# Kernel optimization log

Measured on AMD Instinct MI355X. Metric: run time of the kernel, lower is better.

The kernel has to match this reference:

```python
import jax, jax.numpy as jnp
import numpy as np

V = 8192
E = 262144
IN_DIM = 128
OUT_DIM = 128
NEG_SLOPE = 0.2


def setup_inputs() -> dict:
    key = jax.random.key(0)
    k1, k2, k3, k4 = jax.random.split(key, 4)
    h = jax.random.normal(k1, (V, IN_DIM), dtype=jnp.float32)
    edge_index = jax.random.randint(k2, (2, E), 0, V, dtype=jnp.int64)
    # nn.Linear weights: W (out_dim, in_dim), att (1, 2*out_dim), both bias-free
    W = jax.random.normal(k3, (OUT_DIM, IN_DIM), dtype=jnp.float32) / np.sqrt(IN_DIM)
    att_w = jax.random.normal(k4, (1, 2 * OUT_DIM), dtype=jnp.float32) / np.sqrt(2 * OUT_DIM)
    return {"h": h, "edge_index": edge_index, "W": W, "att_w": att_w}


def reference(h, edge_index, W, att_w):
    # h: (V, in_dim) -> (V, out_dim)
    hw = h @ W.T
    src, dst = edge_index[0], edge_index[1]
    # edge features: concat of endpoint embeddings -> (E, 2*out_dim)
    e = jnp.concatenate([hw[src], hw[dst]], axis=-1)
    # attention logits per edge, LeakyReLU(0.2)
    a = jax.nn.leaky_relu(jnp.squeeze(e @ att_w.T, -1), negative_slope=NEG_SLOPE)
    v = hw.shape[0]
    # faithful to original: dense V x V matrix, zeros on non-edges,
    # softmax over ALL columns (non-edges included as score 0)
    alpha = jnp.zeros((v, v), dtype=hw.dtype).at[src, dst].set(a)
    alpha = jax.nn.softmax(alpha, axis=-1)
    # dropout is identity in eval mode (deterministic reference)
    return alpha @ hw
```

## Files before the change

kernel.cpp:

```cpp
#include <hip/hip_runtime.h>
#include <hip/hip_bf16.h>
#include <math.h>


#define V 8192
#define E 262144
#define D 128
#define NEG_SLOPE 0.2f
#define CAP 96
#define CSTRIDE 16
#define HWB 512

#define FMA4(acc, hv, wv) { acc.x += (hv)*(wv).x; acc.y += (hv)*(wv).y; \
                            acc.z += (hv)*(wv).z; acc.w += (hv)*(wv).w; }

__device__ __forceinline__ unsigned short f2bf(float f) {
    unsigned u = __float_as_uint(f);
    return (unsigned short)((u + 0x7fffu + ((u >> 16) & 1u)) >> 16);
}
__device__ __forceinline__ float bf2f_low(int p) {
    return __uint_as_float(((unsigned)p) << 16);
}

__global__ __launch_bounds__(256) void k_hw(const float* __restrict__ h,
                                            const float* __restrict__ W,
                                            const float* __restrict__ att,
                                            unsigned short* __restrict__ hwb,
                                            float* __restrict__ s1,
                                            float* __restrict__ s2,
                                            float* __restrict__ Pb,
                                            int* __restrict__ cnt) {
    __shared__ float Wt[D * 132];
    __shared__ float atts[2 * D];
    __shared__ float scr[8 * D];
    int t = threadIdx.x, b = blockIdx.x;
    int g = b * 256 + t;
    cnt[g] = 0;
    atts[t] = att[t];
    for (int f = t; f < D * D; f += 256) {
        int o = f >> 7, k = f & 127;
        Wt[k * 132 + o] = W[f];
    }
    __syncthreads();

    int c4 = (t & 31) * 4;
    int rq = t >> 5;
    int r0 = b * 16;
    float4 a0 = make_float4(0.f,0.f,0.f,0.f), a1 = a0;
    const float* h0p = &h[(r0 + rq    ) * D];
    const float* h1p = &h[(r0 + rq + 8) * D];
    #pragma unroll 4
    for (int kq = 0; kq < D; kq += 4) {
        float4 w0 = *(const float4*)&Wt[(kq + 0) * 132 + c4];
        float4 w1 = *(const float4*)&Wt[(kq + 1) * 132 + c4];
        float4 w2 = *(const float4*)&Wt[(kq + 2) * 132 + c4];
        float4 w3 = *(const float4*)&Wt[(kq + 3) * 132 + c4];
        float4 hv;
        hv = *(const float4*)&h0p[kq];
        FMA4(a0, hv.x, w0); FMA4(a0, hv.y, w1); FMA4(a0, hv.z, w2); FMA4(a0, hv.w, w3);
        hv = *(const float4*)&h1p[kq];
        FMA4(a1, hv.x, w0); FMA4(a1, hv.y, w1); FMA4(a1, hv.z, w2); FMA4(a1, hv.w, w3);
    }
    *(ushort4*)&hwb[(r0 + rq    ) * D + c4] = make_ushort4(f2bf(a0.x), f2bf(a0.y), f2bf(a0.z), f2bf(a0.w));
    *(ushort4*)&hwb[(r0 + rq + 8) * D + c4] = make_ushort4(f2bf(a1.x), f2bf(a1.y), f2bf(a1.z), f2bf(a1.w));

    float q1a = a0.x * atts[c4] + a0.y * atts[c4 + 1] + a0.z * atts[c4 + 2] + a0.w * atts[c4 + 3];
    float q2a = a0.x * atts[D + c4] + a0.y * atts[D + c4 + 1] + a0.z * atts[D + c4 + 2] + a0.w * atts[D + c4 + 3];
    float q1b = a1.x * atts[c4] + a1.y * atts[c4 + 1] + a1.z * atts[c4 + 2] + a1.w * atts[c4 + 3];
    float q2b = a1.x * atts[D + c4] + a1.y * atts[D + c4 + 1] + a1.z * atts[D + c4 + 2] + a1.w * atts[D + c4 + 3];
    #pragma unroll
    for (int m = 16; m; m >>= 1) {
        q1a += __shfl_xor(q1a, m);
        q2a += __shfl_xor(q2a, m);
        q1b += __shfl_xor(q1b, m);
        q2b += __shfl_xor(q2b, m);
    }
    if ((t & 31) == 0) {
        s1[r0 + rq    ] = q1a;
        s2[r0 + rq    ] = q2a;
        s1[r0 + rq + 8] = q1b;
        s2[r0 + rq + 8] = q2b;
    }

    *(float4*)&scr[rq * D + c4] = make_float4(a0.x + a1.x, a0.y + a1.y,
                                              a0.z + a1.z, a0.w + a1.w);
    __syncthreads();
    if (t < D) {
        float s = 0.f;
        #pragma unroll
        for (int r = 0; r < 8; ++r) s += scr[r * D + t];
        Pb[b * D + t] = s;
    }
}

__global__ __launch_bounds__(256) void k_scatter(const int* __restrict__ ei,
                                                 const float* __restrict__ s1,
                                                 const float* __restrict__ s2,
                                                 int* __restrict__ cnt,
                                                 int* __restrict__ bucket,
                                                 const float* __restrict__ Pb,
                                                 float* __restrict__ S) {
    int b = blockIdx.x, t = threadIdx.x;
    if (b < 1024) {
        int g = b * 256 + t;
        int src = ei[g];
        int dst = ei[E + g];
        float a = s1[src] + s2[dst];
        a = a > 0.f ? a : NEG_SLOPE * a;
        float w = expf(a) - 1.f;
        int pos = atomicAdd(&cnt[src * CSTRIDE], 1);
        if (pos < CAP)
            bucket[src * CAP + pos] = (dst << 16) | (int)f2bf(w);
    } else {
        __shared__ float red[256];
        int bb = b - 1024;
        int c = bb * 32 + (t & 31);
        int rg = t >> 5;
        float s = 0.f;
        #pragma unroll 4
        for (int r = rg; r < HWB; r += 8)
            s += Pb[r * D + c];
        red[t] = s;
        __syncthreads();
        if (t < 32) {
            float v = red[t] + red[t + 32] + red[t + 64] + red[t + 96]
                    + red[t + 128] + red[t + 160] + red[t + 192] + red[t + 224];
            S[bb * 32 + t] = v;
        }
    }
}

__global__ __launch_bounds__(256) void k_row(const int* __restrict__ bucket,
                                             const int* __restrict__ cnt,
                                             const unsigned short* __restrict__ hwb,
                                             const float* __restrict__ S,
                                             float* __restrict__ out) {
    __shared__ int lb[4][CAP];
    __shared__ unsigned bm[4][256];
    int t = threadIdx.x;
    int wv = t >> 6, lane = t & 63;
    int row = blockIdx.x * 4 + wv;
    int deg = cnt[row * CSTRIDE];
    if (deg > CAP) deg = CAP;
    *(uint4*)&bm[wv][lane * 4] = make_uint4(0u, 0u, 0u, 0u);
    const int* bk = bucket + row * CAP;
    int e0 = bk[lane];
    int e1 = (lane < CAP - 64) ? bk[64 + lane] : 0;
    int p0 = (lane < deg)      ? e0 : 0;
    int p1 = (64 + lane < deg) ? e1 : 0;
    if (lane < deg) {
        unsigned d = (unsigned)p0 >> 16;
        unsigned m = 1u << (d & 31);
        if (atomicOr(&bm[wv][d >> 5], m) & m) p0 &= ~0xFFFF;
    }
    if (64 + lane < deg) {
        unsigned d = (unsigned)p1 >> 16;
        unsigned m = 1u << (d & 31);
        if (atomicOr(&bm[wv][d >> 5], m) & m) p1 &= ~0xFFFF;
    }
    lb[wv][lane] = p0;
    if (lane < CAP - 64) lb[wv][64 + lane] = p1;
    int n0 = deg < 64 ? deg : 64;
    float accx = 0.f, accy = 0.f, dex = 0.f;
    const int* myb = lb[wv];
    int col2 = lane * 2;
    int j = 0;
    for (; j + 8 <= n0; j += 8) {
        int4 pa = *(const int4*)&myb[j];
        int4 pb = *(const int4*)&myb[j + 4];
        int da0 = pa.x >> 16, da1 = pa.y >> 16, da2 = pa.z >> 16, da3 = pa.w >> 16;
        int db0 = pb.x >> 16, db1 = pb.y >> 16, db2 = pb.z >> 16, db3 = pb.w >> 16;
        unsigned ha0 = *(const unsigned*)&hwb[da0 * D + col2];
        unsigned ha1 = *(const unsigned*)&hwb[da1 * D + col2];
        unsigned ha2 = *(const unsigned*)&hwb[da2 * D + col2];
        unsigned ha3 = *(const unsigned*)&hwb[da3 * D + col2];
        unsigned hb0 = *(const unsigned*)&hwb[db0 * D + col2];
        unsigned hb1 = *(const unsigned*)&hwb[db1 * D + col2];
        unsigned hb2 = *(const unsigned*)&hwb[db2 * D + col2];
        unsigned hb3 = *(const unsigned*)&hwb[db3 * D + col2];
        float wa0 = bf2f_low(pa.x);
        float wa1 = bf2f_low(pa.y);
        float wa2 = bf2f_low(pa.z);
        float wa3 = bf2f_low(pa.w);
        float wb0 = bf2f_low(pb.x);
        float wb1 = bf2f_low(pb.y);
        float wb2 = bf2f_low(pb.z);
        float wb3 = bf2f_low(pb.w);
        accx += wa0 * __uint_as_float(ha0 << 16);
        accy += wa0 * __uint_as_float(ha0 & 0xFFFF0000u);
        accx += wa1 * __uint_as_float(ha1 << 16);
        accy += wa1 * __uint_as_float(ha1 & 0xFFFF0000u);
        accx += wa2 * __uint_as_float(ha2 << 16);
        accy += wa2 * __uint_as_float(ha2 & 0xFFFF0000u);
        accx += wa3 * __uint_as_float(ha3 << 16);
        accy += wa3 * __uint_as_float(ha3 & 0xFFFF0000u);
        accx += wb0 * __uint_as_float(hb0 << 16);
        accy += wb0 * __uint_as_float(hb0 & 0xFFFF0000u);
        accx += wb1 * __uint_as_float(hb1 << 16);
        accy += wb1 * __uint_as_float(hb1 & 0xFFFF0000u);
        accx += wb2 * __uint_as_float(hb2 << 16);
        accy += wb2 * __uint_as_float(hb2 & 0xFFFF0000u);
        accx += wb3 * __uint_as_float(hb3 << 16);
        accy += wb3 * __uint_as_float(hb3 & 0xFFFF0000u);
        dex += wa0 + wa1 + wa2 + wa3 + wb0 + wb1 + wb2 + wb3;
    }
    for (; j < n0; ++j) {
        int pj = myb[j];
        int dj = pj >> 16;
        float wj = bf2f_low(pj);
        unsigned hv = *(const unsigned*)&hwb[dj * D + col2];
        accx += wj * __uint_as_float(hv << 16);
        accy += wj * __uint_as_float(hv & 0xFFFF0000u);
        dex += wj;
    }
    for (j = 64; j < deg; ++j) {
        int pj = myb[j];
        int dj = pj >> 16;
        float wj = bf2f_low(pj);
        unsigned hv = *(const unsigned*)&hwb[dj * D + col2];
        accx += wj * __uint_as_float(hv << 16);
        accy += wj * __uint_as_float(hv & 0xFFFF0000u);
        dex += wj;
    }
    float inv = 1.f / ((float)V + dex);
    float2 s = *(const float2*)&S[col2];
    float2 o;
    o.x = (s.x + accx) * inv;
    o.y = (s.y + accy) * inv;
    *(float2*)&out[row * D + col2] = o;
}

extern "C" void kernel_launch(void* const* d_in, const int* in_sizes, int n_in,
                              void* d_out, int out_size, void* d_ws, size_t ws_size,
                              hipStream_t stream) {
    const float* h   = (const float*)d_in[0];
    const int*   ei  = (const int*)d_in[1];
    const float* W   = (const float*)d_in[2];
    const float* att = (const float*)d_in[3];
    float* out = (float*)d_out;

    char* ws = (char*)d_ws;
    unsigned short* hwb = (unsigned short*)(ws);
    float* s1  = (float*)(ws + 2097152);
    float* s2  = (float*)(ws + 2129920);
    float* S   = (float*)(ws + 2162688);
    int*   cnt = (int*)(ws + 2163200);
    int*   bucket = (int*)(ws + 2687488);
    float* Pb  = (float*)(ws + 5833216);

    k_hw     <<<HWB,  256, 0, stream>>>(h, W, att, hwb, s1, s2, Pb, cnt);
    k_scatter<<<1028, 256, 0, stream>>>(ei, s1, s2, cnt, bucket, Pb, S);
    k_row    <<<2048, 256, 0, stream>>>(bucket, cnt, hwb, S, out);
}
```

Before: 97.07 us.

## Remap hw matmul threads per wave and split gather across half-waves

The projection kernel now gives each 64-lane wave four rows with two columns per lane, replacing eight 32-lane groups that each handled two rows with four columns per lane. Each lane reads W as float2 from a narrower padded LDS tile and does a full 64-lane attention-score reduction. The aggregation kernel splits each wave into two halves that take even and odd edges, each lane gathering 8-byte (4 bf16) chunks, and the halves are combined with one cross-half shuffle. This aims to halve the number of gather instructions per row and remove the tail loops, by padding the edge count to a multiple of 8. It relies on the padded bucket slots being zeroed so they contribute nothing.

Result: slower. 102.6 us (+5.7%).

```diff
diff --git a/kernel.cpp b/kernel.cpp
--- a/kernel.cpp
+++ b/kernel.cpp
@@ -10,9 +10,6 @@
 #define CAP 96
 #define CSTRIDE 16
 #define HWB 512
-
-#define FMA4(acc, hv, wv) { acc.x += (hv)*(wv).x; acc.y += (hv)*(wv).y; \
-                            acc.z += (hv)*(wv).z; acc.w += (hv)*(wv).w; }
 
 __device__ __forceinline__ unsigned short f2bf(float f) {
     unsigned u = __float_as_uint(f);
@@ -30,65 +27,92 @@
                                             float* __restrict__ s2,
                                             float* __restrict__ Pb,
                                             int* __restrict__ cnt) {
-    __shared__ float Wt[D * 132];
+    __shared__ float Wt[D * 130];
     __shared__ float atts[2 * D];
-    __shared__ float scr[8 * D];
+    __shared__ float scr[4 * D];
     int t = threadIdx.x, b = blockIdx.x;
     int g = b * 256 + t;
     cnt[g] = 0;
     atts[t] = att[t];
     for (int f = t; f < D * D; f += 256) {
         int o = f >> 7, k = f & 127;
-        Wt[k * 132 + o] = W[f];
+        Wt[k * 130 + o] = W[f];
     }
     __syncthreads();
 
-    int c4 = (t & 31) * 4;
-    int rq = t >> 5;
-    int r0 = b * 16;
-    float4 a0 = make_float4(0.f,0.f,0.f,0.f), a1 = a0;
-    const float* h0p = &h[(r0 + rq    ) * D];
-    const float* h1p = &h[(r0 + rq + 8) * D];
+    int l = t & 63;
+    int ww = t >> 6;
+    int c2 = l * 2;
+    int r0 = b * 16 + ww * 4;
+    float2 a0 = make_float2(0.f, 0.f), a1 = a0, a2 = a0, a3 = a0;
+    const float* h0p = &h[(r0 + 0) * D];
+    const float* h1p = &h[(r0 + 1) * D];
+    const float* h2p = &h[(r0 + 2) * D];
+    const float* h3p = &h[(r0 + 3) * D];
     #pragma unroll 4
     for (int kq = 0; kq < D; kq += 4) {
-        float4 w0 = *(const float4*)&Wt[(kq + 0) * 132 + c4];
-        float4 w1 = *(const float4*)&Wt[(kq + 1) * 132 + c4];
-        float4 w2 = *(const float4*)&Wt[(kq + 2) * 132 + c4];
-        float4 w3 = *(const float4*)&Wt[(kq + 3) * 132 + c4];
+        float2 w0 = *(const float2*)&Wt[(kq + 0) * 130 + c2];
+        float2 w1 = *(const float2*)&Wt[(kq + 1) * 130 + c2];
+        float2 w2 = *(const float2*)&Wt[(kq + 2) * 130 + c2];
+        float2 w3 = *(const float2*)&Wt[(kq + 3) * 130 + c2];
         float4 hv;
         hv = *(const float4*)&h0p[kq];
-        FMA4(a0, hv.x, w0); FMA4(a0, hv.y, w1); FMA4(a0, hv.z, w2); FMA4(a0, hv.w, w3);
+        a0.x += hv.x*w0.x; a0.y += hv.x*w0.y;
+        a0.x += hv.y*w1.x; a0.y += hv.y*w1.y;
+        a0.x += hv.z*w2.x; a0.y += hv.z*w2.y;
+        a0.x += hv.w*w3.x; a0.y += hv.w*w3.y;
         hv = *(const float4*)&h1p[kq];
-        FMA4(a1, hv.x, w0); FMA4(a1, hv.y, w1); FMA4(a1, hv.z, w2); FMA4(a1, hv.w, w3);
-    }
-    *(ushort4*)&hwb[(r0 + rq    ) * D + c4] = make_ushort4(f2bf(a0.x), f2bf(a0.y), f2bf(a0.z), f2bf(a0.w));
-    *(ushort4*)&hwb[(r0 + rq + 8) * D + c4] = make_ushort4(f2bf(a1.x), f2bf(a1.y), f2bf(a1.z), f2bf(a1.w));
-
-    float q1a = a0.x * atts[c4] + a0.y * atts[c4 + 1] + a0.z * atts[c4 + 2] + a0.w * atts[c4 + 3];
-    float q2a = a0.x * atts[D + c4] + a0.y * atts[D + c4 + 1] + a0.z * atts[D + c4 + 2] + a0.w * atts[D + c4 + 3];
-    float q1b = a1.x * atts[c4] + a1.y * atts[c4 + 1] + a1.z * atts[c4 + 2] + a1.w * atts[c4 + 3];
-    float q2b = a1.x * atts[D + c4] + a1.y * atts[D + c4 + 1] + a1.z * atts[D + c4 + 2] + a1.w * atts[D + c4 + 3];
+        a1.x += hv.x*w0.x; a1.y += hv.x*w0.y;
+        a1.x += hv.y*w1.x; a1.y += hv.y*w1.y;
+        a1.x += hv.z*w2.x; a1.y += hv.z*w2.y;
+        a1.x += hv.w*w3.x; a1.y += hv.w*w3.y;
+        hv = *(const float4*)&h2p[kq];
+        a2.x += hv.x*w0.x; a2.y += hv.x*w0.y;
+        a2.x += hv.y*w1.x; a2.y += hv.y*w1.y;
+        a2.x += hv.z*w2.x; a2.y += hv.z*w2.y;
+        a2.x += hv.w*w3.x; a2.y += hv.w*w3.y;
+        hv = *(const float4*)&h3p[kq];
+        a3.x += hv.x*w0.x; a3.y += hv.x*w0.y;
+        a3.x += hv.y*w1.x; a3.y += hv.y*w1.y;
+        a3.x += hv.z*w2.x; a3.y += hv.z*w2.y;
+        a3.x += hv.w*w3.x; a3.y += hv.w*w3.y;
+    }
+    *(ushort2*)&hwb[(r0 + 0) * D + c2] = make_ushort2(f2bf(a0.x), f2bf(a0.y));
+    *(ushort2*)&hwb[(r0 + 1) * D + c2] = make_ushort2(f2bf(a1.x), f2bf(a1.y));
+    *(ushort2*)&hwb[(r0 + 2) * D + c2] = make_ushort2(f2bf(a2.x), f2bf(a2.y));
+    *(ushort2*)&hwb[(r0 + 3) * D + c2] = make_ushort2(f2bf(a3.x), f2bf(a3.y));
+
+    float q1_0 = a0.x * atts[c2] + a0.y * atts[c2 + 1];
+    float q2_0 = a0.x * atts[D + c2] + a0.y * atts[D + c2 + 1];
+    float q1_1 = a1.x * atts[c2] + a1.y * atts[c2 + 1];
+    float q2_1 = a1.x * atts[D + c2] + a1.y * atts[D + c2 + 1];
+    float q1_2 = a2.x * atts[c2] + a2.y * atts[c2 + 1];
+    float q2_2 = a2.x * atts[D + c2] + a2.y * atts[D + c2 + 1];
+    float q1_3 = a3.x * atts[c2] + a3.y * atts[c2 + 1];
+    float q2_3 = a3.x * atts[D + c2] + a3.y * atts[D + c2 + 1];
     #pragma unroll
-    for (int m = 16; m; m >>= 1) {
-        q1a += __shfl_xor(q1a, m);
-        q2a += __shfl_xor(q2a, m);
-        q1b += __shfl_xor(q1b, m);
-        q2b += __shfl_xor(q2b, m);
-    }
-    if ((t & 31) == 0) {
-        s1[r0 + rq    ] = q1a;
-        s2[r0 + rq    ] = q2a;
-        s1[r0 + rq + 8] = q1b;
-        s2[r0 + rq + 8] = q2b;
-    }
-
-    *(float4*)&scr[rq * D + c4] = make_float4(a0.x + a1.x, a0.y + a1.y,
-                                              a0.z + a1.z, a0.w + a1.w);
+    for (int m = 32; m; m >>= 1) {
+        q1_0 += __shfl_xor(q1_0, m);
+        q2_0 += __shfl_xor(q2_0, m);
+        q1_1 += __shfl_xor(q1_1, m);
+        q2_1 += __shfl_xor(q2_1, m);
+        q1_2 += __shfl_xor(q1_2, m);
+        q2_2 += __shfl_xor(q2_2, m);
+        q1_3 += __shfl_xor(q1_3, m);
+        q2_3 += __shfl_xor(q2_3, m);
+    }
+    if (l == 0) {
+        s1[r0 + 0] = q1_0;  s2[r0 + 0] = q2_0;
+        s1[r0 + 1] = q1_1;  s2[r0 + 1] = q2_1;
+        s1[r0 + 2] = q1_2;  s2[r0 + 2] = q2_2;
+        s1[r0 + 3] = q1_3;  s2[r0 + 3] = q2_3;
+    }
+
+    *(float2*)&scr[ww * D + c2] = make_float2(a0.x + a1.x + a2.x + a3.x,
+                                              a0.y + a1.y + a2.y + a3.y);
     __syncthreads();
     if (t < D) {
-        float s = 0.f;
-        #pragma unroll
-        for (int r = 0; r < 8; ++r) s += scr[r * D + t];
+        float s = scr[t] + scr[D + t] + scr[2 * D + t] + scr[3 * D + t];
         Pb[b * D + t] = s;
     }
 }
@@ -160,74 +184,46 @@
     }
     lb[wv][lane] = p0;
     if (lane < CAP - 64) lb[wv][64 + lane] = p1;
-    int n0 = deg < 64 ? deg : 64;
-    float accx = 0.f, accy = 0.f, dex = 0.f;
     const int* myb = lb[wv];
-    int col2 = lane * 2;
-    int j = 0;
-    for (; j + 8 <= n0; j += 8) {
+    int li = lane & 31, half = lane >> 5;
+    int col4 = li * 4;
+    float ax = 0.f, ay = 0.f, az = 0.f, aw = 0.f, dex = 0.f;
+    int nr = (deg + 7) & ~7;
+
+    #define PROC(EV, OD) { \
+        int ps_ = half ? (OD) : (EV); \
+        int ds_ = ps_ >> 16; \
+        float ws_ = bf2f_low(ps_); \
+        unsigned long long hv_ = *(const unsigned long long*)&hwb[ds_ * D + col4]; \
+        unsigned lo_ = (unsigned)hv_, hi_ = (unsigned)(hv_ >> 32); \
+        ax += ws_ * __uint_as_float(lo_ << 16); \
+        ay += ws_ * __uint_as_float(lo_ & 0xFFFF0000u); \
+        az += ws_ * __uint_as_float(hi_ << 16); \
+        aw += ws_ * __uint_as_float(hi_ & 0xFFFF0000u); \
+        dex += ws_; }
+
+    for (int j = 0; j < nr; j += 8) {
         int4 pa = *(const int4*)&myb[j];
         int4 pb = *(const int4*)&myb[j + 4];
-        int da0 = pa.x >> 16, da1 = pa.y >> 16, da2 = pa.z >> 16, da3 = pa.w >> 16;
-        int db0 = pb.x >> 16, db1 = pb.y >> 16, db2 = pb.z >> 16, db3 = pb.w >> 16;
-        unsigned ha0 = *(const unsigned*)&hwb[da0 * D + col2];
-        unsigned ha1 = *(const unsigned*)&hwb[da1 * D + col2];
-        unsigned ha2 = *(const unsigned*)&hwb[da2 * D + col2];
-        unsigned ha3 = *(const unsigned*)&hwb[da3 * D + col2];
-        unsigned hb0 = *(const unsigned*)&hwb[db0 * D + col2];
-        unsigned hb1 = *(const unsigned*)&hwb[db1 * D + col2];
-        unsigned hb2 = *(const unsigned*)&hwb[db2 * D + col2];
-        unsigned hb3 = *(const unsigned*)&hwb[db3 * D + col2];
-        float wa0 = bf2f_low(pa.x);
-        float wa1 = bf2f_low(pa.y);
-        float wa2 = bf2f_low(pa.z);
-        float wa3 = bf2f_low(pa.w);
-        float wb0 = bf2f_low(pb.x);
-        float wb1 = bf2f_low(pb.y);
-        float wb2 = bf2f_low(pb.z);
-        float wb3 = bf2f_low(pb.w);
-        accx += wa0 * __uint_as_float(ha0 << 16);
-        accy += wa0 * __uint_as_float(ha0 & 0xFFFF0000u);
-        accx += wa1 * __uint_as_float(ha1 << 16);
-        accy += wa1 * __uint_as_float(ha1 & 0xFFFF0000u);
-        accx += wa2 * __uint_as_float(ha2 << 16);
-        accy += wa2 * __uint_as_float(ha2 & 0xFFFF0000u);
-        accx += wa3 * __uint_as_float(ha3 << 16);
-        accy += wa3 * __uint_as_float(ha3 & 0xFFFF0000u);
-        accx += wb0 * __uint_as_float(hb0 << 16);
-        accy += wb0 * __uint_as_float(hb0 & 0xFFFF0000u);
-        accx += wb1 * __uint_as_float(hb1 << 16);
-        accy += wb1 * __uint_as_float(hb1 & 0xFFFF0000u);
-        accx += wb2 * __uint_as_float(hb2 << 16);
-        accy += wb2 * __uint_as_float(hb2 & 0xFFFF0000u);
-        accx += wb3 * __uint_as_float(hb3 << 16);
-        accy += wb3 * __uint_as_float(hb3 & 0xFFFF0000u);
-        dex += wa0 + wa1 + wa2 + wa3 + wb0 + wb1 + wb2 + wb3;
-    }
-    for (; j < n0; ++j) {
-        int pj = myb[j];
-        int dj = pj >> 16;
-        float wj = bf2f_low(pj);
-        unsigned hv = *(const unsigned*)&hwb[dj * D + col2];
-        accx += wj * __uint_as_float(hv << 16);
-        accy += wj * __uint_as_float(hv & 0xFFFF0000u);
-        dex += wj;
-    }
-    for (j = 64; j < deg; ++j) {
-        int pj = myb[j];
-        int dj = pj >> 16;
-        float wj = bf2f_low(pj);
-        unsigned hv = *(const unsigned*)&hwb[dj * D + col2];
-        accx += wj * __uint_as_float(hv << 16);
-        accy += wj * __uint_as_float(hv & 0xFFFF0000u);
-        dex += wj;
-    }
+        PROC(pa.x, pa.y)
+        PROC(pa.z, pa.w)
+        PROC(pb.x, pb.y)
+        PROC(pb.z, pb.w)
+    }
+    #undef PROC
+
+    ax += __shfl_xor(ax, 32);
+    ay += __shfl_xor(ay, 32);
+    az += __shfl_xor(az, 32);
+    aw += __shfl_xor(aw, 32);
+    dex += __shfl_xor(dex, 32);
     float inv = 1.f / ((float)V + dex);
-    float2 s = *(const float2*)&S[col2];
+    int c = col4 + half * 2;
+    float2 sv = *(const float2*)&S[c];
     float2 o;
-    o.x = (s.x + accx) * inv;
-    o.y = (s.y + accy) * inv;
-    *(float2*)&out[row * D + col2] = o;
+    o.x = ((half ? az : ax) + sv.x) * inv;
+    o.y = ((half ? aw : ay) + sv.y) * inv;
+    *(float2*)&out[row * D + c] = o;
 }
 
 extern "C" void kernel_launch(void* const* d_in, const int* in_sizes, int n_in,
```
